# Kernel optimization log

Measured on AMD Instinct MI355X. Metric: run time of the kernel, lower is better.

## Reference

```python
import jax, jax.numpy as jnp
import numpy as np

N_LABELS = 16
LABEL_DIM = 128
BN_EPS = 1e-5


def setup_inputs() -> dict:
    key = jax.random.key(0)
    k1, k2 = jax.random.split(key, 2)
    B, T, D = 8, 512, 768
    return {
        "features": jax.random.normal(k1, (B, T, D), dtype=jnp.float32),
        "mask": jnp.ones((B, T), dtype=bool),
        "bn_gamma": jnp.ones((D,), dtype=jnp.float32),
        "bn_beta": jnp.zeros((D,), dtype=jnp.float32),
        "ff_w": jax.random.normal(k2, (LABEL_DIM * N_LABELS * 2, D), dtype=jnp.float32) * 0.02,
        "ff_b": jnp.zeros((LABEL_DIM * N_LABELS * 2,), dtype=jnp.float32),
        "label_bias": jnp.zeros((N_LABELS,), dtype=jnp.float32),
    }


def reference(features, mask, bn_gamma, bn_beta, ff_w, ff_b, label_bias):
    B, T, D = features.shape
    m = mask.astype(features.dtype)[..., None]  # [B,T,1]
    denom = jnp.maximum(m.sum(), 1.0)
    # FlatBatchNorm (training mode): stats over masked tokens, zeros elsewhere
    mean = (features * m).sum(axis=(0, 1)) / denom
    var = (((features - mean) ** 2) * m).sum(axis=(0, 1)) / denom
    normed = (features - mean) * jax.lax.rsqrt(var + BN_EPS) * bn_gamma + bn_beta
    feats = normed * m  # res[mask]=flat, zeros elsewhere
    # FFN + relu -> [B,T,n_labels,label_dim,2]
    h = jax.nn.relu(jnp.einsum('btd,od->bto', feats, ff_w) + ff_b)
    h = h.reshape(B, T, N_LABELS, LABEL_DIM, 2)
    start_f = h[..., 0]  # [B,T,L,D]
    end_f = h[..., 1]
    # biaffine span scores: [B, L, T_start, T_end]
    scores = jnp.einsum('bsld,beld->blse', start_f, end_f) + label_bias[None, :, None, None]
    triu = jnp.triu(jnp.ones((T, T), dtype=bool))
    spans_mask = triu[None, None] & mask[:, None, :, None] & mask[:, None, None, :]  # [B,L,T,T] via broadcast
    spans_mask = jnp.broadcast_to(spans_mask, scores.shape)
    return scores, spans_mask
```

## Files before the change

kernel.cpp:

```cpp
#include <hip/hip_runtime.h>

#define B_    8
#define T_    512
#define D_    768
#define L_    16
#define DL_   128
#define NO_   4096
#define M_    4096
#define BN_EPS 1e-5f

typedef __attribute__((ext_vector_type(8))) short short8;
typedef __attribute__((ext_vector_type(4))) float f32x4;
typedef __attribute__((ext_vector_type(2))) float f32x2;

__device__ inline unsigned short f2bf(float x) {
    unsigned int u = __float_as_uint(x);
    unsigned int r = (u + 0x7fffu + ((u >> 16) & 1u)) >> 16;
    return (unsigned short)r;
}

__device__ __forceinline__ void gload_lds16(const unsigned short* g, unsigned short* l) {
    __builtin_amdgcn_global_load_lds(
        (const __attribute__((address_space(1))) unsigned int*)g,
        (__attribute__((address_space(3))) unsigned int*)l, 16, 0, 0);
}

__global__ void k_stats(const float* __restrict__ f, const int* __restrict__ mask,
                        float* __restrict__ stats) {
    int tid = threadIdx.x;
    int t0  = blockIdx.x * 16;
    float s0 = 0.f, s1 = 0.f, s2 = 0.f, q0 = 0.f, q1 = 0.f, q2 = 0.f;
    for (int tt = 0; tt < 16; ++tt) {
        int t = t0 + tt;
        float m = mask[t] ? 1.f : 0.f;
        const float* row = f + (size_t)t * D_;
        float x0 = row[tid];
        float x1 = row[tid + 256];
        float x2 = row[tid + 512];
        s0 += x0 * m; q0 += x0 * x0 * m;
        s1 += x1 * m; q1 += x1 * x1 * m;
        s2 += x2 * m; q2 += x2 * x2 * m;
    }
    atomicAdd(&stats[tid      ], s0);
    atomicAdd(&stats[tid + 256], s1);
    atomicAdd(&stats[tid + 512], s2);
    atomicAdd(&stats[768 + tid      ], q0);
    atomicAdd(&stats[768 + tid + 256], q1);
    atomicAdd(&stats[768 + tid + 512], q2);
    if (tid == 0) {
        int c = 0;
        for (int tt = 0; tt < 16; ++tt) c += (mask[t0 + tt] ? 1 : 0);
        atomicAdd(&stats[1536], (float)c);
    }
}

__global__ void k_normcast(const float4* __restrict__ f4, const float4* __restrict__ w4,
                           const int* __restrict__ mask, const float* __restrict__ stats,
                           const float* __restrict__ gamma, const float* __restrict__ beta,
                           unsigned short* __restrict__ featp, unsigned short* __restrict__ wp) {
    int i = blockIdx.x * 256 + threadIdx.x;
    if (i < M_ * D_ / 4) {
        int d4 = i % (D_ / 4);
        int t  = i / (D_ / 4);
        float m = mask[t] ? 1.f : 0.f;
        float4 v = f4[i];
        int d = d4 * 4;
        float denom = fmaxf(stats[1536], 1.f);
        float sc[4], sh[4];
#pragma unroll
        for (int c = 0; c < 4; ++c) {
            float mean = stats[d + c] / denom;
            float var  = fmaxf(stats[768 + d + c] / denom - mean * mean, 0.f);
            float s    = gamma[d + c] * rsqrtf(var + BN_EPS);
            sc[c] = s;
            sh[c] = beta[d + c] - mean * s;
        }
        float r0 = (v.x * sc[0] + sh[0]) * m;
        float r1 = (v.y * sc[1] + sh[1]) * m;
        float r2 = (v.z * sc[2] + sh[2]) * m;
        float r3 = (v.w * sc[3] + sh[3]) * m;
        ushort4 o;
        o.x = f2bf(r0); o.y = f2bf(r1); o.z = f2bf(r2); o.w = f2bf(r3);
        ((ushort4*)featp)[i] = o;
    } else {
        int j = i - M_ * D_ / 4;
        float4 v = w4[j];
        ushort4 o;
        o.x = f2bf(v.x); o.y = f2bf(v.y); o.z = f2bf(v.z); o.w = f2bf(v.w);
        ((ushort4*)wp)[j] = o;
    }
}

__launch_bounds__(512, 2)
__global__ void k_ffn(const unsigned short* __restrict__ A, const unsigned short* __restrict__ W,
                      const float* __restrict__ bias,
                      unsigned short* __restrict__ startp, unsigned short* __restrict__ endp) {
    __shared__ alignas(16) unsigned short LA[4][8192];
    __shared__ alignas(16) unsigned short LB[4][8192];
    int h   = blockIdx.x;
    int xcd = h & 7, q = h >> 3;
    int bm  = xcd * 4 + (q >> 5);
    int bn  = q & 31;
    int tid  = threadIdx.x;
    int wave = tid >> 6, lane = tid & 63;
    int wm = wave >> 2, wn = wave & 3;
    int lr = lane & 15, quad = lane >> 4;
    int srow = lane >> 3;
    int sg   = (lane & 7) ^ srow;
    const unsigned short* asrc[2];
    const unsigned short* bsrc[2];
#pragma unroll
    for (int p = 0; p < 2; ++p) {
        int c = wave * 2 + p;
        asrc[p] = A + (size_t)(bm * 128 + c * 8 + srow) * D_ + sg * 8;
        bsrc[p] = W + (size_t)(bn * 128 + c * 8 + srow) * D_ + sg * 8;
    }
    int aoff[4][2], boff[2][2];
#pragma unroll
    for (int i = 0; i < 4; ++i)
#pragma unroll
        for (int kk = 0; kk < 2; ++kk) {
            int row = wm * 64 + i * 16 + lr;
            aoff[i][kk] = row * 64 + ((kk * 4 + quad) ^ (row & 7)) * 8;
        }
#pragma unroll
    for (int j = 0; j < 2; ++j)
#pragma unroll
        for (int kk = 0; kk < 2; ++kk) {
            int row = wn * 32 + j * 16 + lr;
            boff[j][kk] = row * 64 + ((kk * 4 + quad) ^ (row & 7)) * 8;
        }
    f32x4 acc[4][2] = {};
#pragma unroll
    for (int t = 0; t < 2; ++t) {
#pragma unroll
        for (int p = 0; p < 2; ++p) {
            int c = wave * 2 + p;
            gload_lds16(asrc[p] + t * 64, &LA[t][c * 512]);
            gload_lds16(bsrc[p] + t * 64, &LB[t][c * 512]);
        }
    }
#pragma unroll
    for (int t = 0; t < 12; ++t) {
        if (t == 11) asm volatile("s_waitcnt vmcnt(0)\ns_barrier" ::: "memory");
        else         asm volatile("s_waitcnt vmcnt(4)\ns_barrier" ::: "memory");
        const unsigned short* la = LA[t & 3];
        const unsigned short* lb = LB[t & 3];
        short8 af[4][2], bf[2][2];
#pragma unroll
        for (int i = 0; i < 4; ++i)
#pragma unroll
            for (int kk = 0; kk < 2; ++kk)
                af[i][kk] = *(const short8*)&la[aoff[i][kk]];
#pragma unroll
        for (int j = 0; j < 2; ++j)
#pragma unroll
            for (int kk = 0; kk < 2; ++kk)
                bf[j][kk] = *(const short8*)&lb[boff[j][kk]];
        if (t < 10) {
            int ss = (t + 2) & 3;
            int ko = (t + 2) * 64;
#pragma unroll
            for (int p = 0; p < 2; ++p) {
                int c = wave * 2 + p;
                gload_lds16(asrc[p] + ko, &LA[ss][c * 512]);
                gload_lds16(bsrc[p] + ko, &LB[ss][c * 512]);
            }
        }
        __builtin_amdgcn_s_setprio(1);
#pragma unroll
        for (int kk = 0; kk < 2; ++kk)
#pragma unroll
            for (int i = 0; i < 4; ++i)
#pragma unroll
                for (int j = 0; j < 2; ++j)
                    acc[i][j] = __builtin_amdgcn_mfma_f32_16x16x32_bf16(af[i][kk], bf[j][kk], acc[i][j], 0, 0, 0);
        __builtin_amdgcn_s_setprio(0);
    }
    __syncthreads();
    unsigned short* C16 = &LA[0][0];
#pragma unroll
    for (int i = 0; i < 4; ++i) {
#pragma unroll
        for (int j = 0; j < 2; ++j) {
            int col_local = wn * 32 + j * 16 + lr;
            float bv = bias[bn * 128 + col_local];
            int a   = col_local & 1;
            int ddp = col_local >> 1;
#pragma unroll
            for (int r = 0; r < 4; ++r) {
                int row = wm * 64 + i * 16 + quad * 4 + r;
                float v = fmaxf(acc[i][j][r] + bv, 0.f);
                C16[row * 136 + a * 64 + ddp] = f2bf(v);
            }
        }
    }
    __syncthreads();
    int bb     = bm >> 2;
    int l      = bn >> 1;
    int ddbase = (bn & 1) * 64;
#pragma unroll
    for (int it = 0; it < 4; ++it) {
        int flat  = it * 512 + tid;
        int piece = flat & 7;
        int run   = flat >> 3;
        int a     = run & 1;
        int row   = run >> 1;
        int tt    = (bm & 3) * 128 + row;
        uint4 v = *(const uint4*)&C16[row * 136 + a * 64 + piece * 8];
        unsigned short* dst = a ? endp : startp;
        size_t off = ((size_t)(bb * 16 + l) * 512 + tt) * 128 + ddbase + piece * 8;
        *(uint4*)&dst[off] = v;
    }
}

__launch_bounds__(256)
__global__ void k_biaffine(const unsigned short* __restrict__ startp,
                           const unsigned short* __restrict__ endp,
                           const int* __restrict__ mask,
                           const float* __restrict__ lbias,
                           float* __restrict__ out_scores, float* __restrict__ out_mask) {
    __shared__ alignas(16) float smemf[64 * 132];
    unsigned short* As = (unsigned short*)smemf;
    unsigned short* Bs = As + 128 * 64;
    float* Cs = smemf;
    int hgrid = blockIdx.x;
    int xcd = hgrid & 7, q = hgrid >> 3;
    int bl  = xcd * 16 + (q >> 4);
    int inner = q & 15;
    int bm = inner & 3, bn = inner >> 2;
    int b  = bl >> 4;
    int tid = threadIdx.x;
    const unsigned short* A  = startp + (size_t)bl * 512 * 128;
    const unsigned short* Bp = endp   + (size_t)bl * 512 * 128;
    int wave = tid >> 6, lane = tid & 63;
    int wm = wave >> 1, wn = wave & 1;
    int lr = lane & 15, quad = lane >> 4;
    f32x4 acc[4][4] = {};
    int srow = lane >> 3;
    for (int half = 0; half < 2; ++half) {
#pragma unroll
        for (int p = 0; p < 4; ++p) {
            int c   = wave * 4 + p;
            int row = c * 8 + srow;
            int gl  = (lane & 7) ^ (row & 7);
            gload_lds16(A  + (size_t)(bm * 128 + row) * DL_ + half * 64 + gl * 8, &As[c * 512]);
            gload_lds16(Bp + (size_t)(bn * 128 + row) * DL_ + half * 64 + gl * 8, &Bs[c * 512]);
        }
        __syncthreads();
#pragma unroll
        for (int kk = 0; kk < 2; ++kk) {
            short8 a[4], bb[4];
#pragma unroll
            for (int i = 0; i < 4; ++i) {
                int row = wm * 64 + i * 16 + lr;
                int gp  = (kk * 4 + quad) ^ (row & 7);
                a[i] = *(const short8*)&As[row * 64 + gp * 8];
            }
#pragma unroll
            for (int j = 0; j < 4; ++j) {
                int row = wn * 64 + j * 16 + lr;
                int gp  = (kk * 4 + quad) ^ (row & 7);
                bb[j] = *(const short8*)&Bs[row * 64 + gp * 8];
            }
#pragma unroll
            for (int i = 0; i < 4; ++i)
#pragma unroll
                for (int j = 0; j < 4; ++j)
                    acc[i][j] = __builtin_amdgcn_mfma_f32_16x16x32_bf16(a[i], bb[j], acc[i][j], 0, 0, 0);
        }
        __syncthreads();
    }
    float lb = lbias[bl & 15];
    float* obase = out_scores + (size_t)bl * 512 * 512;
    float* mbase = out_mask   + (size_t)bl * 512 * 512;
    int e0 = bn * 128 + lane * 2;
    float me0 = mask[b * 512 + e0    ] ? 1.f : 0.f;
    float me1 = mask[b * 512 + e0 + 1] ? 1.f : 0.f;
    for (int hh = 0; hh < 2; ++hh) {
        if (wm == hh) {
#pragma unroll
            for (int i = 0; i < 4; ++i)
#pragma unroll
                for (int j = 0; j < 4; ++j)
#pragma unroll
                    for (int r = 0; r < 4; ++r)
                        Cs[(i * 16 + quad * 4 + r) * 132 + wn * 64 + j * 16 + lr] = acc[i][j][r];
        }
        __syncthreads();
#pragma unroll
        for (int rr = 0; rr < 16; ++rr) {
            int rloc = wave * 16 + rr;
            int s = bm * 128 + hh * 64 + rloc;
            f32x2 v = *(const f32x2*)&Cs[rloc * 132 + lane * 2];
            v.x += lb; v.y += lb;
            float ms = mask[b * 512 + s] ? 1.f : 0.f;
            f32x2 mk;
            mk.x = (s <= e0    ) ? ms * me0 : 0.f;
            mk.y = (s <= e0 + 1) ? ms * me1 : 0.f;
            size_t off = (size_t)s * 512 + e0;
            __builtin_nontemporal_store(v,  (f32x2*)&obase[off]);
            __builtin_nontemporal_store(mk, (f32x2*)&mbase[off]);
        }
        __syncthreads();
    }
}

extern "C" void kernel_launch(void* const* d_in, const int* in_sizes, int n_in,
                              void* d_out, int out_size, void* d_ws, size_t ws_size,
                              hipStream_t stream) {
    const float* features = (const float*)d_in[0];
    const int*   mask     = (const int*)d_in[1];
    const float* gamma    = (const float*)d_in[2];
    const float* beta     = (const float*)d_in[3];
    const float* ffw      = (const float*)d_in[4];
    const float* ffb      = (const float*)d_in[5];
    const float* lbias    = (const float*)d_in[6];

    float* out_scores = (float*)d_out;
    float* out_mask   = out_scores + (size_t)B_ * L_ * T_ * T_;

    char* ws = (char*)d_ws;
    float*          stats  = (float*)ws;
    unsigned short* feats  = (unsigned short*)(ws + 16384);
    unsigned short* wbf    = (unsigned short*)(ws + 16384 + 6291456);
    unsigned short* startp = (unsigned short*)(ws + 12599296);
    unsigned short* endp   = (unsigned short*)(ws + 29376512);

    hipMemsetAsync(ws, 0, 16384, stream);
    k_stats<<<256, 256, 0, stream>>>(features, mask, stats);
    k_normcast<<<6144, 256, 0, stream>>>((const float4*)features, (const float4*)ffw,
                                         mask, stats, gamma, beta, feats, wbf);
    k_ffn<<<1024, 512, 0, stream>>>(feats, wbf, ffb, startp, endp);
    k_biaffine<<<2048, 256, 0, stream>>>(startp, endp, mask, lbias, out_scores, out_mask);
}
```

Measured before the change: 351.3 us.

## Enlarge FFN GEMM tile to 256x128 and widen biaffine epilogue stores

The FFN GEMM tile grows from 128x128 to 256x128 per block, halving the grid to 512 blocks. Each wave now computes a 64x64 sub-tile, and LDS goes from 4-stage to 3-stage buffering to fit the larger A tile. The goal is better operand reuse and fewer redundant weight loads, at the cost of more registers and fewer blocks to spread across CUs. Separately, the biaffine epilogue now writes 16-byte float4 nontemporal stores instead of 8-byte stores, for wider output-write transactions.

```diff
diff --git a/kernel.cpp b/kernel.cpp
--- a/kernel.cpp
+++ b/kernel.cpp
@@ -95,27 +95,31 @@
 __global__ void k_ffn(const unsigned short* __restrict__ A, const unsigned short* __restrict__ W,
                       const float* __restrict__ bias,
                       unsigned short* __restrict__ startp, unsigned short* __restrict__ endp) {
-    __shared__ alignas(16) unsigned short LA[4][8192];
-    __shared__ alignas(16) unsigned short LB[4][8192];
+    __shared__ alignas(16) unsigned short LA[3][16384];
+    __shared__ alignas(16) unsigned short LB[3][8192];
     int h   = blockIdx.x;
     int xcd = h & 7, q = h >> 3;
-    int bm  = xcd * 4 + (q >> 5);
+    int bm  = xcd * 2 + (q >> 5);
     int bn  = q & 31;
     int tid  = threadIdx.x;
     int wave = tid >> 6, lane = tid & 63;
-    int wm = wave >> 2, wn = wave & 3;
+    int wm = wave >> 1, wn = wave & 1;
     int lr = lane & 15, quad = lane >> 4;
     int srow = lane >> 3;
     int sg   = (lane & 7) ^ srow;
-    const unsigned short* asrc[2];
+    const unsigned short* asrc[4];
     const unsigned short* bsrc[2];
+#pragma unroll
+    for (int p = 0; p < 4; ++p) {
+        int c = wave * 4 + p;
+        asrc[p] = A + (size_t)(bm * 256 + c * 8 + srow) * D_ + sg * 8;
+    }
 #pragma unroll
     for (int p = 0; p < 2; ++p) {
         int c = wave * 2 + p;
-        asrc[p] = A + (size_t)(bm * 128 + c * 8 + srow) * D_ + sg * 8;
         bsrc[p] = W + (size_t)(bn * 128 + c * 8 + srow) * D_ + sg * 8;
     }
-    int aoff[4][2], boff[2][2];
+    int aoff[4][2], boff[4][2];
 #pragma unroll
     for (int i = 0; i < 4; ++i)
 #pragma unroll
@@ -124,48 +128,48 @@
             aoff[i][kk] = row * 64 + ((kk * 4 + quad) ^ (row & 7)) * 8;
         }
 #pragma unroll
-    for (int j = 0; j < 2; ++j)
+    for (int j = 0; j < 4; ++j)
 #pragma unroll
         for (int kk = 0; kk < 2; ++kk) {
-            int row = wn * 32 + j * 16 + lr;
+            int row = wn * 64 + j * 16 + lr;
             boff[j][kk] = row * 64 + ((kk * 4 + quad) ^ (row & 7)) * 8;
         }
-    f32x4 acc[4][2] = {};
+    f32x4 acc[4][4] = {};
 #pragma unroll
     for (int t = 0; t < 2; ++t) {
 #pragma unroll
-        for (int p = 0; p < 2; ++p) {
-            int c = wave * 2 + p;
-            gload_lds16(asrc[p] + t * 64, &LA[t][c * 512]);
-            gload_lds16(bsrc[p] + t * 64, &LB[t][c * 512]);
-        }
+        for (int p = 0; p < 4; ++p)
+            gload_lds16(asrc[p] + t * 64, &LA[t][(wave * 4 + p) * 512]);
+#pragma unroll
+        for (int p = 0; p < 2; ++p)
+            gload_lds16(bsrc[p] + t * 64, &LB[t][(wave * 2 + p) * 512]);
     }
 #pragma unroll
     for (int t = 0; t < 12; ++t) {
         if (t == 11) asm volatile("s_waitcnt vmcnt(0)\ns_barrier" ::: "memory");
-        else         asm volatile("s_waitcnt vmcnt(4)\ns_barrier" ::: "memory");
-        const unsigned short* la = LA[t & 3];
-        const unsigned short* lb = LB[t & 3];
-        short8 af[4][2], bf[2][2];
+        else         asm volatile("s_waitcnt vmcnt(6)\ns_barrier" ::: "memory");
+        const unsigned short* la = LA[t % 3];
+        const unsigned short* lb = LB[t % 3];
+        short8 af[4][2], bf[4][2];
 #pragma unroll
         for (int i = 0; i < 4; ++i)
 #pragma unroll
             for (int kk = 0; kk < 2; ++kk)
                 af[i][kk] = *(const short8*)&la[aoff[i][kk]];
 #pragma unroll
-        for (int j = 0; j < 2; ++j)
+        for (int j = 0; j < 4; ++j)
 #pragma unroll
             for (int kk = 0; kk < 2; ++kk)
                 bf[j][kk] = *(const short8*)&lb[boff[j][kk]];
         if (t < 10) {
-            int ss = (t + 2) & 3;
+            int ss = (t + 2) % 3;
             int ko = (t + 2) * 64;
 #pragma unroll
-            for (int p = 0; p < 2; ++p) {
-                int c = wave * 2 + p;
-                gload_lds16(asrc[p] + ko, &LA[ss][c * 512]);
-                gload_lds16(bsrc[p] + ko, &LB[ss][c * 512]);
-            }
+            for (int p = 0; p < 4; ++p)
+                gload_lds16(asrc[p] + ko, &LA[ss][(wave * 4 + p) * 512]);
+#pragma unroll
+            for (int p = 0; p < 2; ++p)
+                gload_lds16(bsrc[p] + ko, &LB[ss][(wave * 2 + p) * 512]);
         }
         __builtin_amdgcn_s_setprio(1);
 #pragma unroll
@@ -173,7 +177,7 @@
 #pragma unroll
             for (int i = 0; i < 4; ++i)
 #pragma unroll
-                for (int j = 0; j < 2; ++j)
+                for (int j = 0; j < 4; ++j)
                     acc[i][j] = __builtin_amdgcn_mfma_f32_16x16x32_bf16(af[i][kk], bf[j][kk], acc[i][j], 0, 0, 0);
         __builtin_amdgcn_s_setprio(0);
     }
@@ -182,8 +186,8 @@
 #pragma unroll
     for (int i = 0; i < 4; ++i) {
 #pragma unroll
-        for (int j = 0; j < 2; ++j) {
-            int col_local = wn * 32 + j * 16 + lr;
+        for (int j = 0; j < 4; ++j) {
+            int col_local = wn * 64 + j * 16 + lr;
             float bv = bias[bn * 128 + col_local];
             int a   = col_local & 1;
             int ddp = col_local >> 1;
@@ -196,17 +200,17 @@
         }
     }
     __syncthreads();
-    int bb     = bm >> 2;
     int l      = bn >> 1;
     int ddbase = (bn & 1) * 64;
 #pragma unroll
-    for (int it = 0; it < 4; ++it) {
+    for (int it = 0; it < 8; ++it) {
         int flat  = it * 512 + tid;
         int piece = flat & 7;
         int run   = flat >> 3;
         int a     = run & 1;
         int row   = run >> 1;
-        int tt    = (bm & 3) * 128 + row;
+        int tg    = bm * 256 + row;
+        int bb    = tg >> 9, tt = tg & 511;
         uint4 v = *(const uint4*)&C16[row * 136 + a * 64 + piece * 8];
         unsigned short* dst = a ? endp : startp;
         size_t off = ((size_t)(bb * 16 + l) * 512 + tt) * 128 + ddbase + piece * 8;
@@ -274,9 +278,12 @@
     float lb = lbias[bl & 15];
     float* obase = out_scores + (size_t)bl * 512 * 512;
     float* mbase = out_mask   + (size_t)bl * 512 * 512;
-    int e0 = bn * 128 + lane * 2;
-    float me0 = mask[b * 512 + e0    ] ? 1.f : 0.f;
-    float me1 = mask[b * 512 + e0 + 1] ? 1.f : 0.f;
+    int rp   = lane >> 5;
+    int colq = (lane & 31) * 4;
+    int e0   = bn * 128 + colq;
+    float me[4];
+#pragma unroll
+    for (int c = 0; c < 4; ++c) me[c] = mask[b * 512 + e0 + c] ? 1.f : 0.f;
     for (int hh = 0; hh < 2; ++hh) {
         if (wm == hh) {
 #pragma unroll
@@ -289,18 +296,18 @@
         }
         __syncthreads();
 #pragma unroll
-        for (int rr = 0; rr < 16; ++rr) {
-            int rloc = wave * 16 + rr;
+        for (int rr = 0; rr < 8; ++rr) {
+            int rloc = wave * 16 + rr * 2 + rp;
             int s = bm * 128 + hh * 64 + rloc;
-            f32x2 v = *(const f32x2*)&Cs[rloc * 132 + lane * 2];
-            v.x += lb; v.y += lb;
+            f32x4 v = *(const f32x4*)&Cs[rloc * 132 + colq];
+            v[0] += lb; v[1] += lb; v[2] += lb; v[3] += lb;
             float ms = mask[b * 512 + s] ? 1.f : 0.f;
-            f32x2 mk;
-            mk.x = (s <= e0    ) ? ms * me0 : 0.f;
-            mk.y = (s <= e0 + 1) ? ms * me1 : 0.f;
+            f32x4 mk;
+#pragma unroll
+            for (int c = 0; c < 4; ++c) mk[c] = (s <= e0 + c) ? ms * me[c] : 0.f;
             size_t off = (size_t)s * 512 + e0;
-            __builtin_nontemporal_store(v,  (f32x2*)&obase[off]);
-            __builtin_nontemporal_store(mk, (f32x2*)&mbase[off]);
+            __builtin_nontemporal_store(v,  (f32x4*)&obase[off]);
+            __builtin_nontemporal_store(mk, (f32x4*)&mbase[off]);
         }
         __syncthreads();
     }
@@ -331,6 +338,6 @@
     k_stats<<<256, 256, 0, stream>>>(features, mask, stats);
     k_normcast<<<6144, 256, 0, stream>>>((const float4*)features, (const float4*)ffw,
                                          mask, stats, gamma, beta, feats, wbf);
-    k_ffn<<<1024, 512, 0, stream>>>(feats, wbf, ffb, startp, endp);
+    k_ffn<<<512, 512, 0, stream>>>(feats, wbf, ffb, startp, endp);
     k_biaffine<<<2048, 256, 0, stream>>>(startp, endp, mask, lbias, out_scores, out_mask);
 }
```

Measured after the change: 338.6 us (median of 2 runs). 3.6% less time.
